# Kernel tuning notes

Measured on AMD Instinct MI355X. Metric: run time of the kernel, lower is better.

The kernel has to match this reference:

```python
import jax, jax.numpy as jnp
import numpy as np

D = 11           # num_classes + 1 (embedding dim)
HL = 7           # window height = 1 + 2*H_PAD
WL = 7           # window width  = 1 + 2*W_PAD
PAD = 3
MAXH, MAXW = 30, 30
FF = 64          # dim_feedforward
EPS = 1e-5       # LayerNorm eps (torch default)
PAD_VALUE = 0.0


def setup_inputs() -> dict:
    key = jax.random.key(0)
    ks = jax.random.split(key, 6)
    N, C, H, W = 1, 10, 16, 16
    s = 0.1
    return {
        "x": jax.random.uniform(ks[0], (N, C, H, W), jnp.float32),
        "Wqkv": jax.random.normal(ks[1], (3 * D, D), jnp.float32) * s,  # in_proj_weight
        "Wo": jax.random.normal(ks[2], (D, D), jnp.float32) * s,        # out_proj.weight
        "W1": jax.random.normal(ks[3], (FF, D), jnp.float32) * s,       # linear1.weight
        "W2": jax.random.normal(ks[4], (D, FF), jnp.float32) * s,       # linear2.weight
        "ln1_w": jnp.ones((D,), jnp.float32),                           # norm1.weight (bias=False)
        "ln2_w": jnp.ones((D,), jnp.float32),                           # norm2.weight (bias=False)
    }


def _layer_norm(x, w):
    m = jnp.mean(x, axis=-1, keepdims=True)
    v = jnp.mean(jnp.square(x - m), axis=-1, keepdims=True)
    return (x - m) / jnp.sqrt(v + EPS) * w


def _encoder_layer(x, Wqkv, Wo, W1, W2, ln1_w, ln2_w):
    # x: [B, S, D]; post-norm, 1 head, no biases, eval mode (dropout off)
    qkv = x @ Wqkv.T
    q, k, v = jnp.split(qkv, 3, axis=-1)
    scale = 1.0 / jnp.sqrt(jnp.float32(D))
    attn = jax.nn.softmax(jnp.einsum('bqd,bkd->bqk', q, k) * scale, axis=-1)
    sa = jnp.einsum('bqk,bkd->bqd', attn, v) @ Wo.T
    x = _layer_norm(x + sa, ln1_w)
    ff = jax.nn.relu(x @ W1.T) @ W2.T
    return _layer_norm(x + ff, ln2_w)


def reference(x, Wqkv, Wo, W1, W2, ln1_w, ln2_w):
    N, C, H, W = x.shape
    C1 = C + 1
    # mask channel: 1 in the padded border, 0 inside
    mask = jnp.pad(jnp.zeros((N, 1, H, W), x.dtype),
                   ((0, 0), (0, 0), (PAD, PAD), (PAD, PAD)), constant_values=1.0)
    xp = jnp.pad(x, ((0, 0), (0, 0), (PAD, PAD), (PAD, PAD)), constant_values=PAD_VALUE)
    xp = jnp.concatenate([xp, mask], axis=1)            # [N, C+1, H+6, W+6]
    win = jnp.stack([xp[:, :, i:i + H, j:j + W]
                     for i in range(HL) for j in range(WL)], axis=-1)  # [N, C1, H, W, 49]
    win = jnp.transpose(win, (0, 2, 3, 1, 4))           # [N, H, W, C1, 49]
    win = win.reshape(N * H * W * C1, HL, WL)
    # embed window into max_height x max_width canvas (rest = pad_value)
    canvas = jnp.full((N * H * W * C1, MAXH, MAXW), PAD_VALUE, x.dtype)
    canvas = canvas.at[:, :HL, :WL].set(win)
    seq = canvas.reshape(N * H * W, C1, MAXH * MAXW).transpose(0, 2, 1)  # [B, S=900, D=11]
    out = _encoder_layer(seq, Wqkv, Wo, W1, W2, ln1_w, ln2_w)
    return out.transpose(0, 2, 1)[:, :-1]               # [B, C, 900]
```

## Files before the change

kernel.cpp:

```cpp
#include <hip/hip_runtime.h>


#define D 11
#define ROWP 12
#define NW 49
#define NWP 52
#define NR 50
#define SEQ 900
#define FFD 64
#define CIN 10
#define NB 256
#define TPB 576
#define NRD (NR * D)
#define TROW 52

__device__ __forceinline__ float dot12(const float4* a, const float4* b) {
    float4 s = make_float4(0.f, 0.f, 0.f, 0.f);
    #pragma unroll
    for (int i = 0; i < 3; ++i) {
        float4 x = a[i], y = b[i];
        s.x += x.x * y.x; s.y += x.y * y.y; s.z += x.z * y.z; s.w += x.w * y.w;
    }
    return s.x + s.y + s.z + s.w;
}

__global__ __launch_bounds__(TPB) void pve_rows(
    const float* __restrict__ gx,
    const float* __restrict__ gWqkv,
    const float* __restrict__ gWo,
    const float* __restrict__ gW1,
    const float* __restrict__ gW2,
    const float* __restrict__ gln1,
    const float* __restrict__ gln2,
    float* __restrict__ T)
{
    __shared__ __align__(16) float sQ[33 * ROWP];
    __shared__ __align__(16) float sWo[D * ROWP];
    __shared__ __align__(16) float sW1[FFD * ROWP];
    __shared__ __align__(16) float sW2[D * FFD];
    __shared__ float sln1[D], sln2[D];
    __shared__ __align__(16) float sSeq[NR][ROWP];
    __shared__ __align__(16) float sK[NW][ROWP];
    __shared__ __align__(16) float sVt[D][NWP];
    __shared__ __align__(16) float sQr[NR][ROWP];
    __shared__ __align__(16) float sE[NR][NWP];
    __shared__ __align__(16) float sNum[NR][ROWP];
    __shared__ float sDen[NR];
    __shared__ __align__(16) float sX1[NR][ROWP];
    __shared__ __align__(16) float sX1n[NR][ROWP];
    __shared__ __align__(16) float sH[NR][FFD];
    __shared__ __align__(16) float sY[NR][ROWP];

    const int tid = threadIdx.x;
    const int b = blockIdx.x;
    const int h = b >> 4;
    const int w = b & 15;

    const int rd = tid;
    const int r = rd / D;
    const int d = rd - r * D;

    for (int i = tid; i < 33 * ROWP; i += TPB) {
        const int rr = i / ROWP, cc = i - rr * ROWP;
        sQ[i] = (cc < D) ? gWqkv[rr * D + cc] : 0.f;
    }
    for (int i = tid; i < D * ROWP; i += TPB) {
        const int rr = i / ROWP, cc = i - rr * ROWP;
        sWo[i] = (cc < D) ? gWo[rr * D + cc] : 0.f;
    }
    for (int i = tid; i < FFD * ROWP; i += TPB) {
        const int rr = i / ROWP, cc = i - rr * ROWP;
        sW1[i] = (cc < D) ? gW1[rr * D + cc] : 0.f;
    }
    for (int i = tid; i < D * FFD; i += TPB) sW2[i] = gW2[i];
    if (tid < D) { sln1[tid] = gln1[tid]; sln2[tid] = gln2[tid]; }

    if (rd < NRD) {
        float val = 0.0f;
        if (r < NW) {
            const int i = r / 7, j = r - (r / 7) * 7;
            const int y = h + i, xx = w + j;
            const bool inter = (y >= 3) && (y < 19) && (xx >= 3) && (xx < 19);
            const int base = inter ? ((y - 3) * 16 + (xx - 3)) : 0;
            if (d < CIN) val = inter ? gx[d * 256 + base] : 0.0f;
            else         val = inter ? 0.0f : 1.0f;
        }
        sSeq[r][d] = val;
        if (d == CIN) sSeq[r][D] = 0.f;
    }
    __syncthreads();

    if (rd < NRD) {
        const float4* sv = (const float4*)&sSeq[r][0];
        const float aq = dot12(sv, (const float4*)&sQ[d * ROWP]);
        const float ak = dot12(sv, (const float4*)&sQ[(D + d) * ROWP]);
        const float av = dot12(sv, (const float4*)&sQ[(2 * D + d) * ROWP]);
        sQr[r][d] = aq;
        if (d == CIN) sQr[r][D] = 0.f;
        if (r < NW) { sK[r][d] = ak; sVt[d][r] = av;
                      if (d == CIN) sK[r][D] = 0.f; }
        else { sVt[d][NW] = 0.f; sVt[d][NW + 1] = 0.f; sVt[d][NW + 2] = 0.f; }
    }
    __syncthreads();

    {
        const float scale = 0.30151134457776363f;
        #pragma unroll
        for (int k = 0; k < 5; ++k) {
            const int idx = tid + k * TPB;
            if (idx < NR * NWP) {
                const int rr = idx / NWP;
                const int tt = idx - rr * NWP;
                float e = 0.f;
                if (tt < NW) {
                    const float s = dot12((const float4*)&sQr[rr][0],
                                          (const float4*)&sK[tt][0]);
                    e = __expf(s * scale);
                }
                sE[rr][tt] = e;
            }
        }
    }
    __syncthreads();

    if (rd < NRD) {
        const float4* ev = (const float4*)&sE[r][0];
        const float4* vv = (const float4*)&sVt[d][0];
        float4 an = make_float4(0.f, 0.f, 0.f, 0.f);
        float4 ad = make_float4(0.f, 0.f, 0.f, 0.f);
        #pragma unroll
        for (int i = 0; i < 13; ++i) {
            const float4 e = ev[i], v = vv[i];
            an.x += e.x * v.x; an.y += e.y * v.y;
            an.z += e.z * v.z; an.w += e.w * v.w;
            ad.x += e.x; ad.y += e.y; ad.z += e.z; ad.w += e.w;
        }
        sNum[r][d] = an.x + an.y + an.z + an.w;
        if (d == CIN) sNum[r][D] = 0.f;
        if (d == 0) sDen[r] = 851.0f + ad.x + ad.y + ad.z + ad.w;
    }
    __syncthreads();

    if (rd < NRD) {
        const float acc = dot12((const float4*)&sNum[r][0],
                                (const float4*)&sWo[d * ROWP]);
        sX1[r][d] = sSeq[r][d] + acc / sDen[r];
        if (d == CIN) sX1[r][D] = 0.f;
    }
    __syncthreads();

    if (rd < NRD) {
        const float4* xv = (const float4*)&sX1[r][0];
        float4 s4 = make_float4(0.f, 0.f, 0.f, 0.f);
        float4 q4 = make_float4(0.f, 0.f, 0.f, 0.f);
        #pragma unroll
        for (int i = 0; i < 3; ++i) {
            const float4 x = xv[i];
            s4.x += x.x; s4.y += x.y; s4.z += x.z; s4.w += x.w;
            q4.x += x.x * x.x; q4.y += x.y * x.y;
            q4.z += x.z * x.z; q4.w += x.w * x.w;
        }
        const float sum = s4.x + s4.y + s4.z + s4.w;
        const float sq  = q4.x + q4.y + q4.z + q4.w;
        const float m   = sum * (1.0f / 11.0f);
        const float var = sq * (1.0f / 11.0f) - m * m;
        sX1n[r][d] = (sX1[r][d] - m) * rsqrtf(var + 1e-5f) * sln1[d];
        if (d == CIN) sX1n[r][D] = 0.f;
    }
    __syncthreads();

    #pragma unroll
    for (int k = 0; k < 6; ++k) {
        const int idx = tid + k * TPB;
        if (idx < NR * FFD) {
            const int rr = idx >> 6;
            const int ff = idx & 63;
            const float acc = dot12((const float4*)&sX1n[rr][0],
                                    (const float4*)&sW1[ff * ROWP]);
            sH[rr][ff] = fmaxf(acc, 0.0f);
        }
    }
    __syncthreads();

    if (rd < NRD) {
        const float4* hv = (const float4*)&sH[r][0];
        const float4* wv = (const float4*)&sW2[d * FFD];
        float4 a4 = make_float4(0.f, 0.f, 0.f, 0.f);
        #pragma unroll
        for (int i = 0; i < 16; ++i) {
            const float4 hh = hv[i], ww = wv[i];
            a4.x += hh.x * ww.x; a4.y += hh.y * ww.y;
            a4.z += hh.z * ww.z; a4.w += hh.w * ww.w;
        }
        sY[r][d] = sX1n[r][d] + a4.x + a4.y + a4.z + a4.w;
        if (d == CIN) sY[r][D] = 0.f;
    }
    __syncthreads();

    if (rd < NRD) {
        const float4* yv = (const float4*)&sY[r][0];
        float4 s4 = make_float4(0.f, 0.f, 0.f, 0.f);
        float4 q4 = make_float4(0.f, 0.f, 0.f, 0.f);
        #pragma unroll
        for (int i = 0; i < 3; ++i) {
            const float4 y = yv[i];
            s4.x += y.x; s4.y += y.y; s4.z += y.z; s4.w += y.w;
            q4.x += y.x * y.x; q4.y += y.y * y.y;
            q4.z += y.z * y.z; q4.w += y.w * y.w;
        }
        const float sum = s4.x + s4.y + s4.z + s4.w;
        const float sq  = q4.x + q4.y + q4.z + q4.w;
        const float m   = sum * (1.0f / 11.0f);
        const float var = sq * (1.0f / 11.0f) - m * m;
        const float val = (sY[r][d] - m) * rsqrtf(var + 1e-5f) * sln2[d];
        if (d < CIN)
            T[(b * CIN + d) * TROW + r] = val;
    }
}

__global__ __launch_bounds__(256) void pve_write(
    const float* __restrict__ T,
    float4* __restrict__ out4)
{
    const int flat = blockIdx.x * 256 + threadIdx.x;
    const int b   = flat / 2250;
    const int rem = flat - b * 2250;
    const int c   = rem / 225;
    const int s0  = (rem - c * 225) * 4;
    const float* tb = T + (b * CIN + c) * TROW;
    float4 v4;
    float* pv = (float*)&v4;
    #pragma unroll
    for (int u = 0; u < 4; ++u) {
        const int s = s0 + u;
        const int i = s / 30;
        const int j = s - i * 30;
        const int row = (i < 7 && j < 7) ? (i * 7 + j) : NW;
        pv[u] = tb[row];
    }
    out4[flat] = v4;
}

extern "C" void kernel_launch(void* const* d_in, const int* in_sizes, int n_in,
                              void* d_out, int out_size, void* d_ws, size_t ws_size,
                              hipStream_t stream) {
    (void)in_sizes; (void)n_in; (void)out_size; (void)ws_size;
    const float* x    = (const float*)d_in[0];
    const float* Wqkv = (const float*)d_in[1];
    const float* Wo   = (const float*)d_in[2];
    const float* W1   = (const float*)d_in[3];
    const float* W2   = (const float*)d_in[4];
    const float* ln1  = (const float*)d_in[5];
    const float* ln2  = (const float*)d_in[6];
    float* T = (float*)d_ws;
    pve_rows<<<NB, TPB, 0, stream>>>(x, Wqkv, Wo, W1, W2, ln1, ln2, T);
    pve_write<<<576000 / 256, 256, 0, stream>>>(T, (float4*)d_out);
}
```

Before: 81.29 us.

## Split each pixel's rows across two blocks to double grid size

Each pixel's 50 unique query rows are now divided between two blocks of 320 threads, giving a grid of 512 smaller blocks instead of 256 large ones. Every block still recomputes the full K and V for its 49 window rows but only handles Q, attention, and FFN for its 25 rows. The aim is more blocks in flight across the CUs and less shared memory per block. The price is duplicated weight loading and K/V projection in each of the paired blocks.

```diff
diff --git a/kernel.cpp b/kernel.cpp
--- a/kernel.cpp
+++ b/kernel.cpp
@@ -9,9 +9,12 @@
 #define SEQ 900
 #define FFD 64
 #define CIN 10
-#define NB 256
-#define TPB 576
+#define RPB 25
+#define GRID_A 512
+#define TPB 320
 #define NRD (NR * D)
+#define NWD (NW * D)
+#define RPD (RPB * D)
 #define TROW 52
 
 __device__ __forceinline__ float dot12(const float4* a, const float4* b) {
@@ -42,23 +45,21 @@
     __shared__ __align__(16) float sSeq[NR][ROWP];
     __shared__ __align__(16) float sK[NW][ROWP];
     __shared__ __align__(16) float sVt[D][NWP];
-    __shared__ __align__(16) float sQr[NR][ROWP];
-    __shared__ __align__(16) float sE[NR][NWP];
-    __shared__ __align__(16) float sNum[NR][ROWP];
-    __shared__ float sDen[NR];
-    __shared__ __align__(16) float sX1[NR][ROWP];
-    __shared__ __align__(16) float sX1n[NR][ROWP];
-    __shared__ __align__(16) float sH[NR][FFD];
-    __shared__ __align__(16) float sY[NR][ROWP];
+    __shared__ __align__(16) float sQr[RPB][ROWP];
+    __shared__ __align__(16) float sE[RPB][NWP];
+    __shared__ __align__(16) float sNum[RPB][ROWP];
+    __shared__ float sDen[RPB];
+    __shared__ __align__(16) float sX1[RPB][ROWP];
+    __shared__ __align__(16) float sX1n[RPB][ROWP];
+    __shared__ __align__(16) float sH[RPB][FFD];
+    __shared__ __align__(16) float sY[RPB][ROWP];
 
     const int tid = threadIdx.x;
-    const int b = blockIdx.x;
+    const int bp = blockIdx.x;
+    const int b = bp >> 1;
+    const int row0 = (bp & 1) * RPB;
     const int h = b >> 4;
     const int w = b & 15;
-
-    const int rd = tid;
-    const int r = rd / D;
-    const int d = rd - r * D;
 
     for (int i = tid; i < 33 * ROWP; i += TPB) {
         const int rr = i / ROWP, cc = i - rr * ROWP;
@@ -75,31 +76,52 @@
     for (int i = tid; i < D * FFD; i += TPB) sW2[i] = gW2[i];
     if (tid < D) { sln1[tid] = gln1[tid]; sln2[tid] = gln2[tid]; }
 
-    if (rd < NRD) {
-        float val = 0.0f;
-        if (r < NW) {
-            const int i = r / 7, j = r - (r / 7) * 7;
-            const int y = h + i, xx = w + j;
-            const bool inter = (y >= 3) && (y < 19) && (xx >= 3) && (xx < 19);
-            const int base = inter ? ((y - 3) * 16 + (xx - 3)) : 0;
-            if (d < CIN) val = inter ? gx[d * 256 + base] : 0.0f;
-            else         val = inter ? 0.0f : 1.0f;
-        }
-        sSeq[r][d] = val;
-        if (d == CIN) sSeq[r][D] = 0.f;
-    }
-    __syncthreads();
-
-    if (rd < NRD) {
-        const float4* sv = (const float4*)&sSeq[r][0];
-        const float aq = dot12(sv, (const float4*)&sQ[d * ROWP]);
-        const float ak = dot12(sv, (const float4*)&sQ[(D + d) * ROWP]);
-        const float av = dot12(sv, (const float4*)&sQ[(2 * D + d) * ROWP]);
-        sQr[r][d] = aq;
-        if (d == CIN) sQr[r][D] = 0.f;
-        if (r < NW) { sK[r][d] = ak; sVt[d][r] = av;
-                      if (d == CIN) sK[r][D] = 0.f; }
-        else { sVt[d][NW] = 0.f; sVt[d][NW + 1] = 0.f; sVt[d][NW + 2] = 0.f; }
+    #pragma unroll
+    for (int k = 0; k < 2; ++k) {
+        const int idx = tid + k * TPB;
+        if (idx < NRD) {
+            const int r = idx / D;
+            const int d = idx - r * D;
+            float val = 0.0f;
+            if (r < NW) {
+                const int i = r / 7, j = r - (r / 7) * 7;
+                const int y = h + i, xx = w + j;
+                const bool inter = (y >= 3) && (y < 19) && (xx >= 3) && (xx < 19);
+                const int base = inter ? ((y - 3) * 16 + (xx - 3)) : 0;
+                if (d < CIN) val = inter ? gx[d * 256 + base] : 0.0f;
+                else         val = inter ? 0.0f : 1.0f;
+            }
+            sSeq[r][d] = val;
+            if (d == CIN) sSeq[r][D] = 0.f;
+        }
+    }
+    __syncthreads();
+
+    #pragma unroll
+    for (int k = 0; k < 2; ++k) {
+        const int idx = tid + k * TPB;
+        if (idx < NWD) {
+            const int t = idx / D;
+            const int d = idx - t * D;
+            const float4* sv = (const float4*)&sSeq[t][0];
+            const float ak = dot12(sv, (const float4*)&sQ[(D + d) * ROWP]);
+            const float av = dot12(sv, (const float4*)&sQ[(2 * D + d) * ROWP]);
+            sK[t][d] = ak;
+            if (d == CIN) sK[t][D] = 0.f;
+            sVt[d][t] = av;
+        }
+    }
+    if (tid < RPD) {
+        const int rl = tid / D;
+        const int d = tid - rl * D;
+        const int r = row0 + rl;
+        const float aq = dot12((const float4*)&sSeq[r][0],
+                               (const float4*)&sQ[d * ROWP]);
+        sQr[rl][d] = aq;
+        if (d == CIN) sQr[rl][D] = 0.f;
+    } else if (tid < RPD + D * 3) {
+        const int p = tid - RPD;
+        sVt[p / 3][NW + (p % 3)] = 0.f;
     }
     __syncthreads();
 
@@ -108,23 +130,25 @@
         #pragma unroll
         for (int k = 0; k < 5; ++k) {
             const int idx = tid + k * TPB;
-            if (idx < NR * NWP) {
-                const int rr = idx / NWP;
-                const int tt = idx - rr * NWP;
+            if (idx < RPB * NWP) {
+                const int rl = idx / NWP;
+                const int tt = idx - rl * NWP;
                 float e = 0.f;
                 if (tt < NW) {
-                    const float s = dot12((const float4*)&sQr[rr][0],
+                    const float s = dot12((const float4*)&sQr[rl][0],
                                           (const float4*)&sK[tt][0]);
                     e = __expf(s * scale);
                 }
-                sE[rr][tt] = e;
+                sE[rl][tt] = e;
             }
         }
     }
     __syncthreads();
 
-    if (rd < NRD) {
-        const float4* ev = (const float4*)&sE[r][0];
+    if (tid < RPD) {
+        const int rl = tid / D;
+        const int d = tid - rl * D;
+        const float4* ev = (const float4*)&sE[rl][0];
         const float4* vv = (const float4*)&sVt[d][0];
         float4 an = make_float4(0.f, 0.f, 0.f, 0.f);
         float4 ad = make_float4(0.f, 0.f, 0.f, 0.f);
@@ -135,22 +159,26 @@
             an.z += e.z * v.z; an.w += e.w * v.w;
             ad.x += e.x; ad.y += e.y; ad.z += e.z; ad.w += e.w;
         }
-        sNum[r][d] = an.x + an.y + an.z + an.w;
-        if (d == CIN) sNum[r][D] = 0.f;
-        if (d == 0) sDen[r] = 851.0f + ad.x + ad.y + ad.z + ad.w;
-    }
-    __syncthreads();
-
-    if (rd < NRD) {
-        const float acc = dot12((const float4*)&sNum[r][0],
+        sNum[rl][d] = an.x + an.y + an.z + an.w;
+        if (d == CIN) sNum[rl][D] = 0.f;
+        if (d == 0) sDen[rl] = 851.0f + ad.x + ad.y + ad.z + ad.w;
+    }
+    __syncthreads();
+
+    if (tid < RPD) {
+        const int rl = tid / D;
+        const int d = tid - rl * D;
+        const float acc = dot12((const float4*)&sNum[rl][0],
                                 (const float4*)&sWo[d * ROWP]);
-        sX1[r][d] = sSeq[r][d] + acc / sDen[r];
-        if (d == CIN) sX1[r][D] = 0.f;
-    }
-    __syncthreads();
-
-    if (rd < NRD) {
-        const float4* xv = (const float4*)&sX1[r][0];
+        sX1[rl][d] = sSeq[row0 + rl][d] + acc / sDen[rl];
+        if (d == CIN) sX1[rl][D] = 0.f;
+    }
+    __syncthreads();
+
+    if (tid < RPD) {
+        const int rl = tid / D;
+        const int d = tid - rl * D;
+        const float4* xv = (const float4*)&sX1[rl][0];
         float4 s4 = make_float4(0.f, 0.f, 0.f, 0.f);
         float4 q4 = make_float4(0.f, 0.f, 0.f, 0.f);
         #pragma unroll
@@ -164,26 +192,28 @@
         const float sq  = q4.x + q4.y + q4.z + q4.w;
         const float m   = sum * (1.0f / 11.0f);
         const float var = sq * (1.0f / 11.0f) - m * m;
-        sX1n[r][d] = (sX1[r][d] - m) * rsqrtf(var + 1e-5f) * sln1[d];
-        if (d == CIN) sX1n[r][D] = 0.f;
-    }
-    __syncthreads();
-
-    #pragma unroll
-    for (int k = 0; k < 6; ++k) {
+        sX1n[rl][d] = (sX1[rl][d] - m) * rsqrtf(var + 1e-5f) * sln1[d];
+        if (d == CIN) sX1n[rl][D] = 0.f;
+    }
+    __syncthreads();
+
+    #pragma unroll
+    for (int k = 0; k < 5; ++k) {
         const int idx = tid + k * TPB;
-        if (idx < NR * FFD) {
-            const int rr = idx >> 6;
+        if (idx < RPB * FFD) {
+            const int rl = idx >> 6;
             const int ff = idx & 63;
-            const float acc = dot12((const float4*)&sX1n[rr][0],
+            const float acc = dot12((const float4*)&sX1n[rl][0],
                                     (const float4*)&sW1[ff * ROWP]);
-            sH[rr][ff] = fmaxf(acc, 0.0f);
-        }
-    }
-    __syncthreads();
-
-    if (rd < NRD) {
-        const float4* hv = (const float4*)&sH[r][0];
+            sH[rl][ff] = fmaxf(acc, 0.0f);
+        }
+    }
+    __syncthreads();
+
+    if (tid < RPD) {
+        const int rl = tid / D;
+        const int d = tid - rl * D;
+        const float4* hv = (const float4*)&sH[rl][0];
         const float4* wv = (const float4*)&sW2[d * FFD];
         float4 a4 = make_float4(0.f, 0.f, 0.f, 0.f);
         #pragma unroll
@@ -192,13 +222,15 @@
             a4.x += hh.x * ww.x; a4.y += hh.y * ww.y;
             a4.z += hh.z * ww.z; a4.w += hh.w * ww.w;
         }
-        sY[r][d] = sX1n[r][d] + a4.x + a4.y + a4.z + a4.w;
-        if (d == CIN) sY[r][D] = 0.f;
-    }
-    __syncthreads();
-
-    if (rd < NRD) {
-        const float4* yv = (const float4*)&sY[r][0];
+        sY[rl][d] = sX1n[rl][d] + a4.x + a4.y + a4.z + a4.w;
+        if (d == CIN) sY[rl][D] = 0.f;
+    }
+    __syncthreads();
+
+    if (tid < RPD) {
+        const int rl = tid / D;
+        const int d = tid - rl * D;
+        const float4* yv = (const float4*)&sY[rl][0];
         float4 s4 = make_float4(0.f, 0.f, 0.f, 0.f);
         float4 q4 = make_float4(0.f, 0.f, 0.f, 0.f);
         #pragma unroll
@@ -212,9 +244,9 @@
         const float sq  = q4.x + q4.y + q4.z + q4.w;
         const float m   = sum * (1.0f / 11.0f);
         const float var = sq * (1.0f / 11.0f) - m * m;
-        const float val = (sY[r][d] - m) * rsqrtf(var + 1e-5f) * sln2[d];
+        const float val = (sY[rl][d] - m) * rsqrtf(var + 1e-5f) * sln2[d];
         if (d < CIN)
-            T[(b * CIN + d) * TROW + r] = val;
+            T[(b * CIN + d) * TROW + row0 + rl] = val;
     }
 }
 
@@ -253,6 +285,6 @@
     const float* ln1  = (const float*)d_in[5];
     const float* ln2  = (const float*)d_in[6];
     float* T = (float*)d_ws;
-    pve_rows<<<NB, TPB, 0, stream>>>(x, Wqkv, Wo, W1, W2, ln1, ln2, T);
+    pve_rows<<<GRID_A, TPB, 0, stream>>>(x, Wqkv, Wo, W1, W2, ln1, ln2, T);
     pve_write<<<576000 / 256, 256, 0, stream>>>(T, (float4*)d_out);
 }
```

New measurement: 81.74 us. Within noise of the previous version (+0.6%).
